# Performance work log

Measured on AMD Instinct MI355X. Metric: run time of the kernel, lower is better.

The kernel has to match this reference:

```python
import jax, jax.numpy as jnp
import numpy as np
from jax import lax

B, C, H, W = 16, 256, 64, 64
EXP = 2
C2 = C * EXP  # expanded channels
EPS = 1e-5


def setup_inputs() -> dict:
    key = jax.random.key(0)
    ks = jax.random.split(key, 8)
    def he(k, shape, fan_out):
        return jax.random.normal(k, shape, jnp.float32) * np.sqrt(2.0 / fan_out)
    return {
        "f": jax.random.normal(ks[0], (B, C, H, W), jnp.float32),
        "ln_gamma": jnp.ones((C,), jnp.float32),
        "ln_beta": jnp.zeros((C,), jnp.float32),
        "w_expand": he(ks[1], (C2, C), C2),          # 1x1 conv [out,in]
        "freq_real": jnp.ones((C2,), jnp.float32),
        "freq_imag": jnp.zeros((C2,), jnp.float32),
        "w_poly": he(ks[2], (C2, C2), C2),
        "w_dw": he(ks[3], (C2, 1, 3, 3), 9),          # depthwise 3x3, fan_out=1*3*3
        "w_pw": he(ks[4], (C2, C2), C2),
        "w_final": he(ks[5], (C, C2), C),
    }


def reference(f, ln_gamma, ln_beta, w_expand, freq_real, freq_imag,
              w_poly, w_dw, w_pw, w_final):
    # LayerNorm over channel dim (torch permutes to NHWC, norms last dim)
    mu = jnp.mean(f, axis=1, keepdims=True)
    var = jnp.var(f, axis=1, keepdims=True)
    f1 = (f - mu) * lax.rsqrt(var + EPS)
    f1 = f1 * ln_gamma[None, :, None, None] + ln_beta[None, :, None, None]
    # 1x1 expand
    f2 = jnp.einsum('bchw,oc->bohw', f1, w_expand)
    # FFT2 -> multiply by per-channel complex scalar (r + i*j) -> IFFT2 -> real.
    # Since the filter is constant over all frequencies and f2 is real, this is
    # exactly Re((r+i*j) * f2) = r * f2; freq_imag contributes nothing.
    f4 = f2 * freq_real[None, :, None, None]
    # polymerize 1x1
    f5 = jnp.einsum('bchw,oc->bohw', f4, w_poly)
    # depthwise 3x3, SAME padding
    f6 = lax.conv_general_dilated(
        f5, w_dw, window_strides=(1, 1), padding='SAME',
        dimension_numbers=('NCHW', 'OIHW', 'NCHW'), feature_group_count=C2)
    # pointwise 1x1
    f6 = jnp.einsum('bchw,oc->bohw', f6, w_pw)
    # GELU (exact erf, torch default) gating
    f7 = jax.nn.gelu(f6, approximate=False) * f6
    # 1x1 reduce + residual
    f8 = jnp.einsum('bchw,oc->bohw', f7, w_final)
    return f + f8
```

## Files before the change

kernel.cpp:

```cpp
#include <hip/hip_runtime.h>
#include <hip/hip_bf16.h>
#include <math.h>

#define Bn 16
#define Cc 256
#define Hh 64
#define Ww 64
#define HW 4096
#define C2 512
#define Pp 65536
#define EPSc 1e-5f

typedef __attribute__((ext_vector_type(8))) short short8;
typedef __attribute__((ext_vector_type(4))) float floatx4;

__global__ __launch_bounds__(512)
void combine_weights(const float* __restrict__ w_expand,
                     const float* __restrict__ freq_real,
                     const float* __restrict__ w_poly,
                     const float* __restrict__ gamma,
                     const float* __restrict__ beta,
                     __hip_bfloat16* __restrict__ W1g_b,
                     float* __restrict__ bias1,
                     float* __restrict__ wsum) {
    int o = blockIdx.x;
    int tid = threadIdx.x;
    int c = tid & 255;
    int kh = tid >> 8;
    float acc = 0.f;
    const float* wp = w_poly + (size_t)o * C2 + kh * 256;
    const float* fr = freq_real + kh * 256;
    const float* we = w_expand + (size_t)(kh * 256) * Cc + c;
    for (int m = 0; m < 256; ++m) {
        acc += wp[m] * fr[m] * we[(size_t)m * Cc];
    }
    __shared__ float part[512];
    __shared__ float redB[256];
    __shared__ float redG[256];
    part[tid] = acc;
    __syncthreads();
    if (tid < 256) {
        float a = part[tid] + part[tid + 256];
        float wg = a * gamma[c];
        W1g_b[(size_t)o * Cc + c] = __float2bfloat16(wg);
        redB[c] = a * beta[c];
        redG[c] = wg;
    }
    __syncthreads();
    for (int s = 128; s > 0; s >>= 1) {
        if (tid < s) { redB[tid] += redB[tid + s]; redG[tid] += redG[tid + s]; }
        __syncthreads();
    }
    if (tid == 0) { bias1[o] = redB[0]; wsum[o] = redG[0]; }
}

__device__ inline void cvt4(const float* __restrict__ a,
                            __hip_bfloat16* __restrict__ o, int q) {
    float4 v = *(const float4*)&a[q * 4];
    __hip_bfloat16 r[4];
    r[0] = __float2bfloat16(v.x);
    r[1] = __float2bfloat16(v.y);
    r[2] = __float2bfloat16(v.z);
    r[3] = __float2bfloat16(v.w);
    *(uint2*)&o[q * 4] = *(const uint2*)r;
}

__global__ __launch_bounds__(256)
void prep_weights(const float* __restrict__ w_pw,
                  const float* __restrict__ w_final,
                  const float* __restrict__ w_dw,
                  __hip_bfloat16* __restrict__ w_pw_b,
                  __hip_bfloat16* __restrict__ w_final_b,
                  float* __restrict__ w_dw_p) {
    int i = blockIdx.x * 256 + threadIdx.x;
    if (i < 65536) {
        cvt4(w_pw, w_pw_b, i);
    } else if (i < 98304) {
        cvt4(w_final, w_final_b, i - 65536);
    } else {
        int j = i - 98304;
        if (j < C2 * 12) {
            int k = j / 12, l = j - k * 12;
            w_dw_p[j] = (l < 9) ? w_dw[k * 9 + l] : 0.f;
        }
    }
}

#define XPAD 264

__global__ __launch_bounds__(512, 4)
void gemm1f(const float* __restrict__ f,
            const __hip_bfloat16* __restrict__ W1g_b,
            const float* __restrict__ bias1,
            const float* __restrict__ wsum,
            __hip_bfloat16* __restrict__ f5) {
    __shared__ __hip_bfloat16 As[64 * XPAD];
    __shared__ float redS[32 * 64];
    __shared__ float redQ[32 * 64];
    __shared__ float muS[64];
    __shared__ float rsS[64];

    int flat = blockIdx.x;
    int b = flat >> 6;
    int h = flat & 63;
    int s0 = h * 64;

    int tid = threadIdx.x;
    int x = tid & 15;
    int cg = tid >> 4;

    const float* fb = f + (size_t)b * Cc * HW + s0 + x * 4;
    unsigned* Asu = (unsigned*)&As[0];

    float lsum[4] = {0.f, 0.f, 0.f, 0.f};
    float lsq[4]  = {0.f, 0.f, 0.f, 0.f};
#pragma unroll
    for (int i = 0; i < 4; ++i) {
        int cp = i * 32 + cg;
        float4 v0 = *(const float4*)&fb[(size_t)(cp * 2) * HW];
        float4 v1 = *(const float4*)&fb[(size_t)(cp * 2 + 1) * HW];
        float a0[4] = {v0.x, v0.y, v0.z, v0.w};
        float a1[4] = {v1.x, v1.y, v1.z, v1.w};
#pragma unroll
        for (int j = 0; j < 4; ++j) {
            lsum[j] += a0[j] + a1[j];
            lsq[j]  += a0[j] * a0[j] + a1[j] * a1[j];
            unsigned pk = ((unsigned)__bfloat16_as_ushort(__float2bfloat16(a1[j])) << 16)
                        |  (unsigned)__bfloat16_as_ushort(__float2bfloat16(a0[j]));
            Asu[(size_t)(x * 4 + j) * (XPAD / 2) + cp] = pk;
        }
    }
#pragma unroll
    for (int j = 0; j < 4; ++j) {
        redS[cg * 64 + x * 4 + j] = lsum[j];
        redQ[cg * 64 + x * 4 + j] = lsq[j];
    }

    int lane = tid & 63, wave = tid >> 6;
    int col = lane & 15, quad = lane >> 4;
    int c0w = wave * 64;
    const __hip_bfloat16* Bp = W1g_b + (size_t)(c0w + col) * Cc + quad * 8;
    short8 B0[4], B1[4];
#pragma unroll
    for (int j = 0; j < 4; ++j) {
        B0[j] = *(const short8*)(Bp + (size_t)j * 16 * Cc);
        B1[j] = *(const short8*)(Bp + (size_t)j * 16 * Cc + 32);
    }

    float ws4[4], bi4[4];
#pragma unroll
    for (int j = 0; j < 4; ++j) {
        int c = c0w + j * 16 + col;
        ws4[j] = wsum[c];
        bi4[j] = bias1[c];
    }

    __syncthreads();
    if (tid < 64) {
        float s = 0.f, q = 0.f;
#pragma unroll
        for (int g = 0; g < 32; ++g) { s += redS[g * 64 + tid]; q += redQ[g * 64 + tid]; }
        float m = s * (1.0f / 256.0f);
        muS[tid] = m;
        rsS[tid] = rsqrtf(q * (1.0f / 256.0f) - m * m + EPSc);
    }
    __syncthreads();

    floatx4 acc[4][4];
#pragma unroll
    for (int i = 0; i < 4; ++i)
#pragma unroll
        for (int j = 0; j < 4; ++j)
            acc[i][j] = (floatx4){0.f, 0.f, 0.f, 0.f};

#pragma unroll
    for (int ks = 0; ks < 8; ++ks) {
        int k0 = ks * 32;
        short8 af[4];
#pragma unroll
        for (int i = 0; i < 4; ++i)
            af[i] = *(const short8*)&As[(size_t)(i * 16 + col) * XPAD + k0 + quad * 8];
        __builtin_amdgcn_s_setprio(1);
#pragma unroll
        for (int i = 0; i < 4; ++i)
#pragma unroll
            for (int j = 0; j < 4; ++j)
                acc[i][j] = __builtin_amdgcn_mfma_f32_16x16x32_bf16(
                    af[i], (ks & 1) ? B1[j] : B0[j], acc[i][j], 0, 0, 0);
        __builtin_amdgcn_s_setprio(0);
        if (ks + 2 < 8) {
#pragma unroll
            for (int j = 0; j < 4; ++j) {
                short8 v = *(const short8*)(Bp + (size_t)j * 16 * Cc + k0 + 64);
                if (ks & 1) B1[j] = v; else B0[j] = v;
            }
        }
    }

    __hip_bfloat16* f5b = f5 + (size_t)b * C2 * HW + s0;
#pragma unroll
    for (int i = 0; i < 4; ++i) {
        int pl = i * 16 + quad * 4;
        float4 mu4 = *(const float4*)&muS[pl];
        float4 rs4 = *(const float4*)&rsS[pl];
        float mu_[4] = {mu4.x, mu4.y, mu4.z, mu4.w};
        float rs_[4] = {rs4.x, rs4.y, rs4.z, rs4.w};
#pragma unroll
        for (int j = 0; j < 4; ++j) {
            int c = c0w + j * 16 + col;
            __hip_bfloat16 v4[4];
#pragma unroll
            for (int r = 0; r < 4; ++r) {
                float v = (acc[i][j][r] - mu_[r] * ws4[j]) * rs_[r] + bi4[j];
                v4[r] = __float2bfloat16(v);
            }
            *(uint2*)&f5b[(size_t)c * HW + pl] = *(const uint2*)v4;
        }
    }
}

#define TPITCH 520

#define P0_LOAD(dst, itc) do {                                               \
    int kk_ = (itc) * 128 + kb;                                              \
    _Pragma("unroll")                                                        \
    for (int dy_ = 0; dy_ < 3; ++dy_) {                                      \
        int hh_ = h + dy_ - 1;                                               \
        if ((unsigned)hh_ < Hh) {                                            \
            const __hip_bfloat16* row_ = f5b + (size_t)kk_ * HW + hh_ * Ww + w16; \
            dst[dy_][0] = *(const uint4*)&row_[0];                           \
            dst[dy_][1] = *(const uint4*)&row_[8];                           \
        } else {                                                             \
            dst[dy_][0] = make_uint4(0, 0, 0, 0);                            \
            dst[dy_][1] = make_uint4(0, 0, 0, 0);                            \
        }                                                                    \
    } } while (0)

__global__ __launch_bounds__(512, 4)
void fused_tail(const __hip_bfloat16* __restrict__ f5,
                const float* __restrict__ w_dw_p,
                const __hip_bfloat16* __restrict__ w_pw_b,
                const __hip_bfloat16* __restrict__ w_final_b,
                const float* __restrict__ f,
                float* __restrict__ out) {
    __shared__ __hip_bfloat16 tT[64 * TPITCH];

    int flat = blockIdx.x;
    int xcd = flat & 7;
    int slot = flat >> 3;
    int hb = slot & 7;
    int b  = slot >> 3;
    int h  = xcd * 8 + hb;

    int tid = threadIdx.x;
    int lane = tid & 63;
    int wave = tid >> 6;
    int col = lane & 15;
    int quad = lane >> 4;

    const __hip_bfloat16* f5b = f5 + (size_t)b * C2 * HW;
    int t4 = tid & 3;
    int kb = tid >> 2;
    int w16 = t4 * 16;

    uint4 bA[3][2], bB[3][2];
    P0_LOAD(bA, 0);
    P0_LOAD(bB, 1);

#pragma unroll
    for (int it = 0; it < 4; ++it) {
        int k = it * 128 + kb;
        const float4* wd4 = (const float4*)(w_dw_p + (size_t)k * 12);
        float4 wa = wd4[0], wb = wd4[1], wc2 = wd4[2];
        float wreg[9] = {wa.x, wa.y, wa.z, wa.w, wb.x, wb.y, wb.z, wb.w, wc2.x};
        float acc16[16] = {};
#pragma unroll
        for (int dy = 0; dy < 3; ++dy) {
            const __hip_bfloat16* pv =
                (const __hip_bfloat16*)((it & 1) ? &bB[dy][0] : &bA[dy][0]);
            float cv[16];
#pragma unroll
            for (int j = 0; j < 16; ++j) cv[j] = __bfloat162float(pv[j]);
            float l_in = __shfl_up(cv[15], 1);
            float r_in = __shfl_down(cv[0], 1);
            if (t4 == 0) l_in = 0.f;
            if (t4 == 3) r_in = 0.f;
            float win[18];
            win[0] = l_in;
#pragma unroll
            for (int j = 0; j < 16; ++j) win[j + 1] = cv[j];
            win[17] = r_in;
#pragma unroll
            for (int j = 0; j < 16; ++j)
                acc16[j] += wreg[dy * 3 + 0] * win[j] +
                            wreg[dy * 3 + 1] * win[j + 1] +
                            wreg[dy * 3 + 2] * win[j + 2];
        }
        if (it + 2 < 4) {
            if (it & 1) { P0_LOAD(bB, it + 2); } else { P0_LOAD(bA, it + 2); }
        }
#pragma unroll
        for (int j = 0; j < 16; ++j)
            tT[(size_t)(w16 + j) * TPITCH + k] = __float2bfloat16(acc16[j]);
    }

    int wm0 = wave * 64;
    const __hip_bfloat16* Ap = w_pw_b + (size_t)(wm0 + col) * C2 + quad * 8;
    short8 A0[4], A1[4];
#pragma unroll
    for (int mt = 0; mt < 4; ++mt)
        A0[mt] = *(const short8*)(Ap + (size_t)mt * 16 * C2);

    __syncthreads();

#pragma unroll
    for (int mt = 0; mt < 4; ++mt)
        A1[mt] = *(const short8*)(Ap + (size_t)mt * 16 * C2 + 32);

    floatx4 acc[4][4];
#pragma unroll
    for (int mt = 0; mt < 4; ++mt)
#pragma unroll
        for (int nt = 0; nt < 4; ++nt)
            acc[mt][nt] = (floatx4){0.f, 0.f, 0.f, 0.f};

#pragma unroll
    for (int ks = 0; ks < 16; ++ks) {
        int k0 = ks * 32;
        short8 bfr[4];
#pragma unroll
        for (int nt = 0; nt < 4; ++nt)
            bfr[nt] = *(const short8*)&tT[(size_t)(nt * 16 + col) * TPITCH + k0 + quad * 8];
        __builtin_amdgcn_s_setprio(1);
#pragma unroll
        for (int mt = 0; mt < 4; ++mt)
#pragma unroll
            for (int nt = 0; nt < 4; ++nt)
                acc[mt][nt] = __builtin_amdgcn_mfma_f32_16x16x32_bf16(
                    (ks & 1) ? A1[mt] : A0[mt], bfr[nt], acc[mt][nt], 0, 0, 0);
        __builtin_amdgcn_s_setprio(0);
        if (ks + 2 < 16) {
#pragma unroll
            for (int mt = 0; mt < 4; ++mt) {
                short8 v = *(const short8*)(Ap + (size_t)mt * 16 * C2 + k0 + 64);
                if (ks & 1) A1[mt] = v; else A0[mt] = v;
            }
        }
    }
    __syncthreads();

#pragma unroll
    for (int mt = 0; mt < 4; ++mt)
#pragma unroll
        for (int nt = 0; nt < 4; ++nt) {
            __hip_bfloat16 v4[4];
#pragma unroll
            for (int r = 0; r < 4; ++r) {
                float v = acc[mt][nt][r];
                float gl = 0.5f * v * (1.0f + erff(v * 0.70710678118f));
                v4[r] = __float2bfloat16(gl * v);
            }
            *(uint2*)&tT[(size_t)(nt * 16 + col) * TPITCH + wm0 + mt * 16 + quad * 4] = *(const uint2*)v4;
        }

    int wm2 = wave * 32;
    const __hip_bfloat16* Af = w_final_b + (size_t)(wm2 + col) * C2 + quad * 8;
    short8 C0[2], C1[2];
#pragma unroll
    for (int mt = 0; mt < 2; ++mt)
        C0[mt] = *(const short8*)(Af + (size_t)mt * 16 * C2);

    const float* fb = f + (size_t)b * Cc * HW + h * Ww;
    float* ob = out + (size_t)b * Cc * HW + h * Ww;
    float fres[2][4][4];
#pragma unroll
    for (int mt = 0; mt < 2; ++mt)
#pragma unroll
        for (int nt = 0; nt < 4; ++nt)
#pragma unroll
            for (int r = 0; r < 4; ++r) {
                int m = wm2 + mt * 16 + quad * 4 + r;
                int n = nt * 16 + col;
                fres[mt][nt][r] = fb[(size_t)m * HW + n];
            }

    __syncthreads();

#pragma unroll
    for (int mt = 0; mt < 2; ++mt)
        C1[mt] = *(const short8*)(Af + (size_t)mt * 16 * C2 + 32);

    floatx4 acc2[2][4];
#pragma unroll
    for (int mt = 0; mt < 2; ++mt)
#pragma unroll
        for (int nt = 0; nt < 4; ++nt)
            acc2[mt][nt] = (floatx4){0.f, 0.f, 0.f, 0.f};

#pragma unroll
    for (int ks = 0; ks < 16; ++ks) {
        int k0 = ks * 32;
        short8 bfr[4];
#pragma unroll
        for (int nt = 0; nt < 4; ++nt)
            bfr[nt] = *(const short8*)&tT[(size_t)(nt * 16 + col) * TPITCH + k0 + quad * 8];
        __builtin_amdgcn_s_setprio(1);
#pragma unroll
        for (int mt = 0; mt < 2; ++mt)
#pragma unroll
            for (int nt = 0; nt < 4; ++nt)
                acc2[mt][nt] = __builtin_amdgcn_mfma_f32_16x16x32_bf16(
                    (ks & 1) ? C1[mt] : C0[mt], bfr[nt], acc2[mt][nt], 0, 0, 0);
        __builtin_amdgcn_s_setprio(0);
        if (ks + 2 < 16) {
#pragma unroll
            for (int mt = 0; mt < 2; ++mt) {
                short8 v = *(const short8*)(Af + (size_t)mt * 16 * C2 + k0 + 64);
                if (ks & 1) C1[mt] = v; else C0[mt] = v;
            }
        }
    }

#pragma unroll
    for (int mt = 0; mt < 2; ++mt)
#pragma unroll
        for (int nt = 0; nt < 4; ++nt)
#pragma unroll
            for (int r = 0; r < 4; ++r) {
                int m = wm2 + mt * 16 + quad * 4 + r;
                int n = nt * 16 + col;
                ob[(size_t)m * HW + n] = fres[mt][nt][r] + acc2[mt][nt][r];
            }
}

extern "C" void kernel_launch(void* const* d_in, const int* in_sizes, int n_in,
                              void* d_out, int out_size, void* d_ws, size_t ws_size,
                              hipStream_t stream) {
    const float* f         = (const float*)d_in[0];
    const float* ln_gamma  = (const float*)d_in[1];
    const float* ln_beta   = (const float*)d_in[2];
    const float* w_expand  = (const float*)d_in[3];
    const float* freq_real = (const float*)d_in[4];
    const float* w_poly    = (const float*)d_in[6];
    const float* w_dw      = (const float*)d_in[7];
    const float* w_pw      = (const float*)d_in[8];
    const float* w_final   = (const float*)d_in[9];
    float* out = (float*)d_out;

    char* p = (char*)d_ws;
    __hip_bfloat16* f5   = (__hip_bfloat16*)p;  p += (size_t)C2 * Pp * 2;
    __hip_bfloat16* W1g_b = (__hip_bfloat16*)p; p += (size_t)C2 * Cc * 2;
    float* bias1 = (float*)p;                   p += (size_t)C2 * 4;
    float* wsum  = (float*)p;                   p += (size_t)C2 * 4;
    __hip_bfloat16* w_pw_b    = (__hip_bfloat16*)p;  p += (size_t)C2 * C2 * 2;
    __hip_bfloat16* w_final_b = (__hip_bfloat16*)p;  p += (size_t)Cc * C2 * 2;
    float* w_dw_p = (float*)p;                  p += (size_t)C2 * 12 * 4;

    combine_weights<<<dim3(C2), dim3(512), 0, stream>>>(
        w_expand, freq_real, w_poly, ln_gamma, ln_beta, W1g_b, bias1, wsum);

    prep_weights<<<dim3(409), dim3(256), 0, stream>>>(
        w_pw, w_final, w_dw, w_pw_b, w_final_b, w_dw_p);

    gemm1f<<<dim3(1024), dim3(512), 0, stream>>>(
        f, W1g_b, bias1, wsum, f5);

    fused_tail<<<dim3(1024), dim3(512), 0, stream>>>(
        f5, w_dw_p, w_pw_b, w_final_b, f, out);
}
```

Before: 343.4 us.

## Stage GEMM outputs through LDS for coalesced stores and swizzle tail LDS layout

gemm1f now writes its normalized bf16 output tile into reused shared memory in two channel halves, then emits 16-byte coalesced row stores to f5 instead of scattered 8-byte stores. fused_tail applies an XOR swizzle to the tT shared buffer indices to reduce bank conflicts. It also stages the final accumulator through LDS so the residual load and output store use float4 coalesced accesses, replacing the per-element fres registers. This adds extra barriers and LDS traffic and raises fused_tail's shared memory, which may lower occupancy.

```diff
diff --git a/kernel.cpp b/kernel.cpp
--- a/kernel.cpp
+++ b/kernel.cpp
@@ -94,11 +94,12 @@
             const float* __restrict__ bias1,
             const float* __restrict__ wsum,
             __hip_bfloat16* __restrict__ f5) {
-    __shared__ __hip_bfloat16 As[64 * XPAD];
-    __shared__ float redS[32 * 64];
-    __shared__ float redQ[32 * 64];
-    __shared__ float muS[64];
-    __shared__ float rsS[64];
+    __shared__ __align__(16) char smem1[50688];
+    __hip_bfloat16* As = (__hip_bfloat16*)smem1;
+    float* redS = (float*)(smem1 + 33792);
+    float* redQ = (float*)(smem1 + 41984);
+    float* muS  = (float*)(smem1 + 50176);
+    float* rsS  = (float*)(smem1 + 50432);
 
     int flat = blockIdx.x;
     int b = flat >> 6;
@@ -197,25 +198,43 @@
         }
     }
 
+    __syncthreads();
+    __hip_bfloat16* Wb = (__hip_bfloat16*)smem1;
     __hip_bfloat16* f5b = f5 + (size_t)b * C2 * HW + s0;
-#pragma unroll
-    for (int i = 0; i < 4; ++i) {
-        int pl = i * 16 + quad * 4;
-        float4 mu4 = *(const float4*)&muS[pl];
-        float4 rs4 = *(const float4*)&rsS[pl];
-        float mu_[4] = {mu4.x, mu4.y, mu4.z, mu4.w};
-        float rs_[4] = {rs4.x, rs4.y, rs4.z, rs4.w};
-#pragma unroll
-        for (int j = 0; j < 4; ++j) {
-            int c = c0w + j * 16 + col;
-            __hip_bfloat16 v4[4];
-#pragma unroll
-            for (int r = 0; r < 4; ++r) {
-                float v = (acc[i][j][r] - mu_[r] * ws4[j]) * rs_[r] + bi4[j];
-                v4[r] = __float2bfloat16(v);
-            }
-            *(uint2*)&f5b[(size_t)c * HW + pl] = *(const uint2*)v4;
-        }
+    int rr = tid >> 3;
+    int rc = tid & 7;
+#pragma unroll
+    for (int chunk = 0; chunk < 2; ++chunk) {
+        if ((wave >> 2) == chunk) {
+            int cbase = c0w & 255;
+#pragma unroll
+            for (int i = 0; i < 4; ++i) {
+                int pl = i * 16 + quad * 4;
+                float4 mu4 = *(const float4*)&muS[pl];
+                float4 rs4 = *(const float4*)&rsS[pl];
+                float mu_[4] = {mu4.x, mu4.y, mu4.z, mu4.w};
+                float rs_[4] = {rs4.x, rs4.y, rs4.z, rs4.w};
+#pragma unroll
+                for (int j = 0; j < 4; ++j) {
+                    int cl = cbase + j * 16 + col;
+                    __hip_bfloat16 v4[4];
+#pragma unroll
+                    for (int r = 0; r < 4; ++r) {
+                        float v = (acc[i][j][r] - mu_[r] * ws4[j]) * rs_[r] + bi4[j];
+                        v4[r] = __float2bfloat16(v);
+                    }
+                    *(uint2*)&Wb[(size_t)cl * 72 + pl] = *(const uint2*)v4;
+                }
+            }
+        }
+        __syncthreads();
+#pragma unroll
+        for (int pass = 0; pass < 4; ++pass) {
+            int cl = pass * 64 + rr;
+            uint4 v = *(const uint4*)&Wb[(size_t)cl * 72 + rc * 8];
+            *(uint4*)&f5b[(size_t)(chunk * 256 + cl) * HW + rc * 8] = v;
+        }
+        if (chunk == 0) __syncthreads();
     }
 }
 
@@ -243,7 +262,9 @@
                 const __hip_bfloat16* __restrict__ w_final_b,
                 const float* __restrict__ f,
                 float* __restrict__ out) {
-    __shared__ __hip_bfloat16 tT[64 * TPITCH];
+    __shared__ __align__(16) char smem[69632];
+    __hip_bfloat16* tT = (__hip_bfloat16*)smem;
+    float* Lf = (float*)smem;
 
     int flat = blockIdx.x;
     int xcd = flat & 7;
@@ -299,9 +320,10 @@
         if (it + 2 < 4) {
             if (it & 1) { P0_LOAD(bB, it + 2); } else { P0_LOAD(bA, it + 2); }
         }
+        int ksw = k ^ (t4 << 4);
 #pragma unroll
         for (int j = 0; j < 16; ++j)
-            tT[(size_t)(w16 + j) * TPITCH + k] = __float2bfloat16(acc16[j]);
+            tT[(size_t)(w16 + j) * TPITCH + ksw] = __float2bfloat16(acc16[j]);
     }
 
     int wm0 = wave * 64;
@@ -330,7 +352,8 @@
         short8 bfr[4];
 #pragma unroll
         for (int nt = 0; nt < 4; ++nt)
-            bfr[nt] = *(const short8*)&tT[(size_t)(nt * 16 + col) * TPITCH + k0 + quad * 8];
+            bfr[nt] = *(const short8*)&tT[(size_t)(nt * 16 + col) * TPITCH +
+                                          ((k0 + quad * 8) ^ (nt << 4))];
         __builtin_amdgcn_s_setprio(1);
 #pragma unroll
         for (int mt = 0; mt < 4; ++mt)
@@ -360,7 +383,8 @@
                 float gl = 0.5f * v * (1.0f + erff(v * 0.70710678118f));
                 v4[r] = __float2bfloat16(gl * v);
             }
-            *(uint2*)&tT[(size_t)(nt * 16 + col) * TPITCH + wm0 + mt * 16 + quad * 4] = *(const uint2*)v4;
+            *(uint2*)&tT[(size_t)(nt * 16 + col) * TPITCH +
+                         ((wm0 + mt * 16 + quad * 4) ^ (nt << 4))] = *(const uint2*)v4;
         }
 
     int wm2 = wave * 32;
@@ -370,20 +394,6 @@
     for (int mt = 0; mt < 2; ++mt)
         C0[mt] = *(const short8*)(Af + (size_t)mt * 16 * C2);
 
-    const float* fb = f + (size_t)b * Cc * HW + h * Ww;
-    float* ob = out + (size_t)b * Cc * HW + h * Ww;
-    float fres[2][4][4];
-#pragma unroll
-    for (int mt = 0; mt < 2; ++mt)
-#pragma unroll
-        for (int nt = 0; nt < 4; ++nt)
-#pragma unroll
-            for (int r = 0; r < 4; ++r) {
-                int m = wm2 + mt * 16 + quad * 4 + r;
-                int n = nt * 16 + col;
-                fres[mt][nt][r] = fb[(size_t)m * HW + n];
-            }
-
     __syncthreads();
 
 #pragma unroll
@@ -403,7 +413,8 @@
         short8 bfr[4];
 #pragma unroll
         for (int nt = 0; nt < 4; ++nt)
-            bfr[nt] = *(const short8*)&tT[(size_t)(nt * 16 + col) * TPITCH + k0 + quad * 8];
+            bfr[nt] = *(const short8*)&tT[(size_t)(nt * 16 + col) * TPITCH +
+                                          ((k0 + quad * 8) ^ (nt << 4))];
         __builtin_amdgcn_s_setprio(1);
 #pragma unroll
         for (int mt = 0; mt < 2; ++mt)
@@ -421,6 +432,7 @@
         }
     }
 
+    __syncthreads();
 #pragma unroll
     for (int mt = 0; mt < 2; ++mt)
 #pragma unroll
@@ -429,8 +441,22 @@
             for (int r = 0; r < 4; ++r) {
                 int m = wm2 + mt * 16 + quad * 4 + r;
                 int n = nt * 16 + col;
-                ob[(size_t)m * HW + n] = fres[mt][nt][r] + acc2[mt][nt][r];
-            }
+                Lf[(size_t)m * 68 + n] = acc2[mt][nt][r];
+            }
+    __syncthreads();
+
+    const float* fb = f + (size_t)b * Cc * HW + h * Ww;
+    float* ob = out + (size_t)b * Cc * HW + h * Ww;
+    int pr = tid >> 4;
+    int pc = tid & 15;
+#pragma unroll
+    for (int pass = 0; pass < 8; ++pass) {
+        int m = pass * 32 + pr;
+        float4 v = *(const float4*)&Lf[(size_t)m * 68 + pc * 4];
+        float4 rr4 = *(const float4*)&fb[(size_t)m * HW + pc * 4];
+        v.x += rr4.x; v.y += rr4.y; v.z += rr4.z; v.w += rr4.w;
+        *(float4*)&ob[(size_t)m * HW + pc * 4] = v;
+    }
 }
 
 extern "C" void kernel_launch(void* const* d_in, const int* in_sizes, int n_in,
```

Result: no change. 337.0 us (-1.9%).
